# Optimization experiments

Hardware: AMD Instinct MI355X
Metric: run time of the kernel (lower is better)

The kernel has to match this reference:

```python
import jax, jax.numpy as jnp
import numpy as np

N = 20000; E = 320000; G = 64; C_IN = 128; H = 128; L = 3; S = 4
EPS = 1e-5; SLOPE = 0.01  # GraphNorm eps, leaky_relu negative slope


def _kruskal(ei, ew, n):
    # Kruskal MST over edges sorted by usage-count weight; returns bidirectional MST edges
    # and the updated usage counts (used edges get +1), mirroring kruskal_mst_track_usage.
    order = np.argsort(ew, kind='stable')
    s = ei[0][order]; d = ei[1][order]
    parent = np.arange(n)
    def find(u):
        while parent[u] != u:
            parent[u] = parent[parent[u]]
            u = parent[u]
        return u
    mst = []; used = []
    for i in range(s.shape[0]):
        ru = find(s[i]); rv = find(d[i])
        if ru != rv:
            parent[ru] = rv
            mst.append((s[i], d[i]))
            used.append(order[i])
            if len(mst) == n - 1:
                break
    ew = ew.copy(); ew[np.asarray(used)] += 1
    m = np.asarray(mst, dtype=np.int64).T  # [2, ~n-1]
    return np.concatenate([m, m[::-1]], axis=1), ew  # bidirectional


def setup_inputs():
    rng = np.random.default_rng(0)
    x = rng.standard_normal((N, C_IN), dtype=np.float32)
    edge_index = rng.integers(0, N, size=(2, E)).astype(np.int64)
    batch = np.sort(rng.integers(0, G, size=N)).astype(np.int64)
    # split_graph: shuffle edges, then repeatedly extract MSTs (no_grad / CPU in original)
    perm = rng.permutation(E)
    ei_p = edge_index[:, perm]
    ew = np.zeros(E, dtype=np.int64)
    msts = []
    for _ in range(S - 1):  # only splits 0..3 are used; split 0 is the shuffled full graph
        m, ew = _kruskal(ei_p, ew, N)
        msts.append(m)
    def gp(shape):
        return jnp.asarray((0.05 * rng.standard_normal(shape)).astype(np.float32))
    return {
        'x': jnp.asarray(x),
        'emb_W': gp((C_IN, H)), 'emb_b': gp((H,)),
        'main_W': gp((L, H, H)), 'main_b': gp((L, H)),
        'main_gw': jnp.ones((L, H), jnp.float32), 'main_gb': jnp.zeros((L, H), jnp.float32), 'main_gms': jnp.ones((L, H), jnp.float32),
        'loc_W': gp((L, H, H)), 'loc_b': gp((L, H)),
        'loc_gw': jnp.ones((L, H), jnp.float32), 'loc_gb': jnp.zeros((L, H), jnp.float32), 'loc_gms': jnp.ones((L, H), jnp.float32),
        'merge_W': gp((H * (S + 1), H)), 'merge_b': gp((H,)),
        'edge_index': jnp.asarray(edge_index),
        'edges0': jnp.asarray(ei_p),
        'edges1': jnp.asarray(msts[0]),
        'edges2': jnp.asarray(msts[1]),
        'edges3': jnp.asarray(msts[2]),
        'batch': jnp.asarray(batch),
    }


def _seg(v, idx, n):
    return jax.ops.segment_sum(v, idx, num_segments=n)


def _gcn(x, W, b, src, dst):
    # PyG GCNConv with self-loops and symmetric normalization
    n = x.shape[0]
    h = x @ W
    deg = _seg(jnp.ones(src.shape[0], x.dtype), dst, n) + 1.0
    dinv = jax.lax.rsqrt(deg)
    coef = (dinv[src] * dinv[dst])[:, None]
    out = _seg(h[src] * coef, dst, n) + h * (dinv * dinv)[:, None]  # neighbors + self-loop
    return out + b


def _graph_norm(x, batch, cnt, w, b, ms):
    # PyG GraphNorm: per-graph mean with learnable mean_scale, per-graph variance
    mean = _seg(x, batch, G) / cnt
    out = x - ms * mean[batch]
    var = _seg(out * out, batch, G) / cnt
    inv = jax.lax.rsqrt(var + EPS)
    return w * out * inv[batch] + b


def _gnn(x, src, dst, Ws, bs, gw, gb, gms, batch, cnt):
    hist = []
    for l in range(L):
        x = _gcn(x, Ws[l], bs[l], src, dst)
        x = _graph_norm(x, batch, cnt, gw[l], gb[l], gms[l])
        x = jax.nn.leaky_relu(x, SLOPE)
        hist.append(x)  # dropout in eval mode = identity
    return hist


def _forward(x, emb_W, emb_b, main_W, main_b, main_gw, main_gb, main_gms,
             loc_W, loc_b, loc_gw, loc_gb, loc_gms, merge_W, merge_b,
             edge_index, edges0, edges1, edges2, edges3, batch):
    cnt = jnp.maximum(_seg(jnp.ones(N, x.dtype), batch, G), 1.0)[:, None]  # [G,1]
    h = x @ emb_W + emb_b
    main_hist = _gnn(h, edge_index[0], edge_index[1], main_W, main_b, main_gw, main_gb, main_gms, batch, cnt)
    split_hists = [_gnn(h, e[0], e[1], loc_W, loc_b, loc_gw, loc_gb, loc_gms, batch, cnt)
                   for e in (edges0, edges1, edges2, edges3)]
    gs = []
    for l in range(L):
        xl = jnp.concatenate([sh[l] for sh in split_hists] + [main_hist[l]], axis=1)  # [N, 5H]
        xl = xl @ merge_W + merge_b
        gs.append(_seg(xl, batch, G) / cnt)  # global_mean_pool
    return jnp.mean(jnp.stack(gs), axis=0)  # [G, H]


def reference(x, emb_W, emb_b, main_W, main_b, main_gw, main_gb, main_gms,
              loc_W, loc_b, loc_gw, loc_gb, loc_gms, merge_W, merge_b,
              edge_index, edges0, edges1, edges2, edges3, batch):
    return _forward(x, emb_W, emb_b, main_W, main_b, main_gw, main_gb, main_gms,
                    loc_W, loc_b, loc_gw, loc_gb, loc_gms, merge_W, merge_b,
                    edge_index, edges0, edges1, edges2, edges3, batch)
```

## Files before the change

kernel.cpp:

```cpp
#include <hip/hip_runtime.h>

#define NN 20000
#define NNP 20032
#define NH 128
#define NG 64
#define NLAY 3
#define NCH 5
#define GEPS 1e-5f
#define GSLOPE 0.01f

typedef unsigned short u16;
typedef unsigned int u32;
typedef __attribute__((ext_vector_type(8))) short short8;
typedef __attribute__((ext_vector_type(4))) float float4v;
typedef __attribute__((ext_vector_type(2))) float f32x2;

__device__ __forceinline__ u16 f2bf(float f) {
  union { float f; u32 u; } v; v.f = f;
  u32 r = (v.u + 0x7fffu + ((v.u >> 16) & 1u)) >> 16;
  return (u16)r;
}

struct ZP {
  const u16* A[NCH];
  const u16* W[NCH];
  u16* Y[NCH];
  int ystride[NCH];
  u16* Xo[NCH];
  u16* Xn[NCH];
  const float* bias[NCH];
  const float* gw[NCH];
  const float* gb[NCH];
  const float* gms[NCH];
  int colbase[NCH];
};

struct ES4 {
  const int* e[4];
  int cnt[4];
  int off[4];
};


__global__ __launch_bounds__(1024) void k_scan(const int* __restrict__ deg,
                                               int* __restrict__ indptr,
                                               int* __restrict__ cursor,
                                               float* __restrict__ dinv,
                                               const int* __restrict__ batch,
                                               int* __restrict__ counts,
                                               int* __restrict__ gstart) {
  int s = blockIdx.x;
  int t = threadIdx.x;
  if (s == 4) {
    int g = t;
    if (g < NG) {
      auto lb = [&](int key) {
        int lo = 0, hi = NN;
        while (lo < hi) {
          int mid = (lo + hi) >> 1;
          if (batch[mid] < key) lo = mid + 1; else hi = mid;
        }
        return lo;
      };
      int a = lb(g), b = lb(g + 1);
      gstart[g] = a;
      counts[g] = b - a;
    }
    return;
  }
  const int* d = deg + s * NN;
  int* ip = indptr + s * (NN + 1);
  int* cu = cursor + s * (NN + 1);
  int lane = t & 63, wv = t >> 6;
  __shared__ int wsum[16];
  int run = 0;
  const int NT = (NN + 1023) / 1024;
  for (int tile = 0; tile < NT; tile++) {
    int idx = tile * 1024 + t;
    int v = 0;
    if (idx < NN) {
      v = d[idx];
      dinv[s * NN + idx] = rsqrtf((float)v + 1.0f);
    }
    int x = v;
#pragma unroll
    for (int o = 1; o < 64; o <<= 1) {
      int y = __shfl_up(x, o);
      if (lane >= o) x += y;
    }
    if (lane == 63) wsum[wv] = x;
    __syncthreads();
    if (wv == 0) {
      int y = (lane < 16) ? wsum[lane] : 0;
#pragma unroll
      for (int o = 1; o < 16; o <<= 1) {
        int z = __shfl_up(y, o);
        if (lane >= o) y += z;
      }
      if (lane < 16) wsum[lane] = y;
    }
    __syncthreads();
    int waveoff = (wv == 0) ? 0 : wsum[wv - 1];
    int excl = run + waveoff + x - v;
    if (idx < NN) { ip[idx] = excl; cu[idx] = excl; }
    run += wsum[15];
    __syncthreads();
  }
  if (t == 0) { ip[NN] = run; cu[NN] = run; }
}

__global__ void k_fill(ES4 es, const float* __restrict__ dinv, int* __restrict__ cursor,
                       u32* __restrict__ ent) {
  int s = blockIdx.y;
  int i = blockIdx.x * 256 + threadIdx.x;
  int E = es.cnt[s];
  if (i >= E) return;
  int src = es.e[s][i];
  int dst = es.e[s][E + i];
  int pos = atomicAdd(&cursor[s * (NN + 1) + dst], 1);
  float c = dinv[s * NN + src] * dinv[s * NN + dst];
  ent[es.off[s] + pos] = (u32)src | ((u32)f2bf(c) << 16);
}

__global__ __launch_bounds__(256) void k_setup(ES4 es, int* __restrict__ deg,
                                               const float* __restrict__ embW,
                                               const float* __restrict__ locW,
                                               const float* __restrict__ mainW,
                                               u16* __restrict__ wt,
                                               const float* __restrict__ x,
                                               u16* __restrict__ xb) {
  int ybk = blockIdx.y;
  if (ybk < 4) {
    int s = ybk;
    int i = blockIdx.x * 256 + threadIdx.x;
    int E = es.cnt[s];
    if (i < E) atomicAdd(&deg[s * NN + es.e[s][E + i]], 1);
    return;
  }
  if (ybk == 11) {
    int i = (blockIdx.x * 256 + threadIdx.x) * 8;
    if (i >= NN * NH) return;
    float4 a = *(const float4*)(x + i);
    float4 b = *(const float4*)(x + i + 4);
    uint4 o;
    o.x = f2bf(a.x) | ((u32)f2bf(a.y) << 16);
    o.y = f2bf(a.z) | ((u32)f2bf(a.w) << 16);
    o.z = f2bf(b.x) | ((u32)f2bf(b.y) << 16);
    o.w = f2bf(b.z) | ((u32)f2bf(b.w) << 16);
    *(uint4*)(xb + i) = o;
    return;
  }
  if (blockIdx.x >= 16) return;
  int mat = ybk - 4;
  const float* W = (mat == 0) ? embW : ((mat <= 3) ? locW + (mat - 1) * NH * NH
                                                   : mainW + (mat - 4) * NH * NH);
  int tile = blockIdx.x;
  int tk = (tile >> 2) * 32;
  int tn = (tile & 3) * 32;
  __shared__ float tl[32][33];
  int c = threadIdx.x & 31, r = threadIdx.x >> 5;
#pragma unroll
  for (int rr = 0; rr < 32; rr += 8)
    tl[r + rr][c] = W[(size_t)(tk + r + rr) * NH + tn + c];
  __syncthreads();
#pragma unroll
  for (int rr = 0; rr < 32; rr += 8)
    wt[(size_t)mat * NH * NH + (size_t)(tn + r + rr) * NH + tk + c] = f2bf(tl[c][r + rr]);
}


__global__ __launch_bounds__(256) void k_gemm_bf(ZP p, const float* __restrict__ gbias) {
  int zi = blockIdx.y;
  const u16* __restrict__ A = p.A[zi];
  const u16* __restrict__ Wt = p.W[zi];
  u16* __restrict__ Y = p.Y[zi];
  int yst = p.ystride[zi];
  __shared__ u16 As[64][136];
  __shared__ u16 Bs[128][136];
  int t = threadIdx.x;
  int row0 = blockIdx.x * 64;
  int c = t & 15, rs = t >> 4;
#pragma unroll
  for (int pass = 0; pass < 4; pass++) {
    int r = pass * 16 + rs;
    *(uint4*)(&As[r][c * 8]) = *(const uint4*)(A + (size_t)(row0 + r) * NH + c * 8);
  }
#pragma unroll
  for (int pass = 0; pass < 8; pass++) {
    int n = pass * 16 + rs;
    *(uint4*)(&Bs[n][c * 8]) = *(const uint4*)(Wt + (size_t)n * NH + c * 8);
  }
  __syncthreads();
  int lane = t & 63, w = t >> 6;
  int m16 = lane & 15, quad = lane >> 4;
  float4v acc[8];
#pragma unroll
  for (int i = 0; i < 8; i++) acc[i] = (float4v)(0.f);
#pragma unroll
  for (int kk = 0; kk < 4; kk++) {
    short8 av = *(const short8*)(&As[w * 16 + m16][kk * 32 + quad * 8]);
#pragma unroll
    for (int ct = 0; ct < 8; ct++) {
      short8 bv = *(const short8*)(&Bs[ct * 16 + m16][kk * 32 + quad * 8]);
      acc[ct] = __builtin_amdgcn_mfma_f32_16x16x32_bf16(av, bv, acc[ct], 0, 0, 0);
    }
  }
  __syncthreads();
#pragma unroll
  for (int ct = 0; ct < 8; ct++) {
    float bv = gbias ? gbias[ct * 16 + m16] : 0.f;
#pragma unroll
    for (int r = 0; r < 4; r++) {
      As[w * 16 + quad * 4 + r][ct * 16 + m16] = f2bf(acc[ct][r] + bv);
    }
  }
  __syncthreads();
#pragma unroll
  for (int pass = 0; pass < 4; pass++) {
    int r = pass * 16 + rs;
    int gr = row0 + r;
    if (gr < NN) *(uint4*)(Y + (size_t)gr * yst + c * 8) = *(const uint4*)(&As[r][c * 8]);
  }
}

__device__ __forceinline__ f32x2 bf2x2(u32 v) {
  f32x2 r;
  r.x = __uint_as_float(v << 16);
  r.y = __uint_as_float(v & 0xffff0000u);
  return r;
}

__device__ __forceinline__ void fma8p(f32x2* a, uint4 v, float cf) {
  f32x2 c2; c2.x = cf; c2.y = cf;
  a[0] += c2 * bf2x2(v.x);
  a[1] += c2 * bf2x2(v.y);
  a[2] += c2 * bf2x2(v.z);
  a[3] += c2 * bf2x2(v.w);
}

__device__ __forceinline__ void fin_chain(const float* a, const u16* Yb, int st, int node,
                                          int fo, float d2, const float* bias,
                                          u16* __restrict__ Xo) {
  uint4 sv = *(const uint4*)(Yb + (size_t)node * st + fo);
  float s[8] = {
    __uint_as_float(sv.x << 16), __uint_as_float(sv.x & 0xffff0000u),
    __uint_as_float(sv.y << 16), __uint_as_float(sv.y & 0xffff0000u),
    __uint_as_float(sv.z << 16), __uint_as_float(sv.z & 0xffff0000u),
    __uint_as_float(sv.w << 16), __uint_as_float(sv.w & 0xffff0000u)};
  float4 b0 = *(const float4*)(bias + fo);
  float4 b1 = *(const float4*)(bias + fo + 4);
  float bb[8] = {b0.x, b0.y, b0.z, b0.w, b1.x, b1.y, b1.z, b1.w};
  float o[8];
#pragma unroll
  for (int j = 0; j < 8; j++) o[j] = a[j] + d2 * s[j] + bb[j];
  uint4 ou;
  u32* op = (u32*)&ou;
#pragma unroll
  for (int j = 0; j < 4; j++)
    op[j] = (u32)f2bf(o[2 * j]) | ((u32)f2bf(o[2 * j + 1]) << 16);
  *(uint4*)(Xo + (size_t)node * NH + fo) = ou;
}

__global__ __launch_bounds__(256) void k_agg2(ZP p, const int* __restrict__ indptr,
                                              const u32* __restrict__ ent,
                                              const float* __restrict__ dinv, int4 entoff) {
  int b = blockIdx.x;
  int wv = threadIdx.x >> 6, lane = threadIdx.x & 63;
  int g = lane >> 4;
  int fo = (lane & 15) * 8;
  if (b < 5000) {
    int node = b * 4 + wv;
    int beg = indptr[node], end = indptr[node + 1];
    const u16* __restrict__ Y0 = p.Y[0];
    const u16* __restrict__ Y4 = p.Y[4];
    int st = p.ystride[0];
    f32x2 a0[4], a4[4];
#pragma unroll
    for (int j = 0; j < 4; j++) { a0[j] = (f32x2)(0.f); a4[j] = (f32x2)(0.f); }
    int e = beg + g;
    for (; e + 4 < end; e += 8) {
      u32 sa = ent[e];
      u32 sb = ent[e + 4];
      size_t ra = (size_t)(sa & 0xffffu) * st + fo;
      size_t rb = (size_t)(sb & 0xffffu) * st + fo;
      uint4 va0 = *(const uint4*)(Y0 + ra);
      uint4 va4 = *(const uint4*)(Y4 + ra);
      uint4 vb0 = *(const uint4*)(Y0 + rb);
      uint4 vb4 = *(const uint4*)(Y4 + rb);
      float ca = __uint_as_float(sa & 0xffff0000u);
      float cb = __uint_as_float(sb & 0xffff0000u);
      fma8p(a0, va0, ca); fma8p(a4, va4, ca);
      fma8p(a0, vb0, cb); fma8p(a4, vb4, cb);
    }
    if (e < end) {
      u32 sc = ent[e];
      float cf = __uint_as_float(sc & 0xffff0000u);
      size_t ro = (size_t)(sc & 0xffffu) * st + fo;
      uint4 v0 = *(const uint4*)(Y0 + ro);
      uint4 v4 = *(const uint4*)(Y4 + ro);
      fma8p(a0, v0, cf);
      fma8p(a4, v4, cf);
    }
    float* f0 = (float*)a0;
    float* f4 = (float*)a4;
#pragma unroll
    for (int j = 0; j < 8; j++) {
      f0[j] += __shfl_xor(f0[j], 16);
      f0[j] += __shfl_xor(f0[j], 32);
      f4[j] += __shfl_xor(f4[j], 16);
      f4[j] += __shfl_xor(f4[j], 32);
    }
    if (g == 0) {
      float di = dinv[node];
      float d2 = di * di;
      fin_chain(f0, Y0, st, node, fo, d2, p.bias[0], p.Xo[0]);
      fin_chain(f4, Y4, st, node, fo, d2, p.bias[4], p.Xo[4]);
    }
  } else {
    int mb = b - 5000;
    int s = 1 + mb / 1250;
    int node = (mb % 1250) * 16 + wv * 4 + g;
    const int* ip = indptr + s * (NN + 1);
    int eb = (s == 1) ? entoff.y : ((s == 2) ? entoff.z : entoff.w);
    const u16* __restrict__ Y = p.Y[s];
    int st = p.ystride[s];
    int beg = ip[node], end = ip[node + 1];
    const u32* __restrict__ ev = ent + eb;
    f32x2 a[4];
#pragma unroll
    for (int j = 0; j < 4; j++) a[j] = (f32x2)(0.f);
    for (int e = beg; e < end; e++) {
      u32 sc = ev[e];
      uint4 v = *(const uint4*)(Y + (size_t)(sc & 0xffffu) * st + fo);
      fma8p(a, v, __uint_as_float(sc & 0xffff0000u));
    }
    float di = dinv[s * NN + node];
    float d2 = di * di;
    fin_chain((float*)a, Y, st, node, fo, d2, p.bias[s], p.Xo[s]);
  }
}

__global__ __launch_bounds__(256) void k_norm2(ZP p, const int* __restrict__ gstart,
                                               const int* __restrict__ counts,
                                               float* __restrict__ Ml) {
  int g = blockIdx.x, zi = blockIdx.y, fc = blockIdx.z;
  const u16* __restrict__ X = p.Xo[zi];
  u16* __restrict__ Xn = p.Xn[zi];
  int t = threadIdx.x;
  int fj = t & 15;
  int f2 = fc * 32 + fj * 2;
  int rh = t >> 4;
  int start = gstart[g], cnt = counts[g];
  __shared__ float red[4][16][17];
  float s0 = 0.f, s1 = 0.f, q0 = 0.f, q1 = 0.f;
  for (int i = rh; i < cnt; i += 16) {
    u32 v = *(const u32*)(X + (size_t)(start + i) * NH + f2);
    float v0 = __uint_as_float(v << 16), v1 = __uint_as_float(v & 0xffff0000u);
    s0 += v0; q0 += v0 * v0;
    s1 += v1; q1 += v1 * v1;
  }
  red[0][rh][fj] = s0; red[1][rh][fj] = s1;
  red[2][rh][fj] = q0; red[3][rh][fj] = q1;
  __syncthreads();
#pragma unroll
  for (int off = 8; off >= 1; off >>= 1) {
    if (rh < off) {
      red[0][rh][fj] += red[0][rh + off][fj];
      red[1][rh][fj] += red[1][rh + off][fj];
      red[2][rh][fj] += red[2][rh + off][fj];
      red[3][rh][fj] += red[3][rh + off][fj];
    }
    __syncthreads();
  }
  float cntf = fmaxf((float)cnt, 1.f);
  float w0 = p.gw[zi][f2], w1 = p.gw[zi][f2 + 1];
  float b0 = p.gb[zi][f2], b1 = p.gb[zi][f2 + 1];
  float ms0 = p.gms[zi][f2], ms1 = p.gms[zi][f2 + 1];
  float mean0 = red[0][0][fj] / cntf, mean1 = red[1][0][fj] / cntf;
  float var0 = red[2][0][fj] / cntf - (2.f * ms0 - ms0 * ms0) * mean0 * mean0;
  float var1 = red[3][0][fj] / cntf - (2.f * ms1 - ms1 * ms1) * mean1 * mean1;
  float inv0 = rsqrtf(var0 + GEPS), inv1 = rsqrtf(var1 + GEPS);
  __syncthreads();
  float m0 = 0.f, m1 = 0.f;
  for (int i = rh; i < cnt; i += 16) {
    size_t ro = (size_t)(start + i) * NH + f2;
    u32 v = *(const u32*)(X + ro);
    float v0 = __uint_as_float(v << 16), v1 = __uint_as_float(v & 0xffff0000u);
    float o0 = w0 * (v0 - ms0 * mean0) * inv0 + b0;
    float o1 = w1 * (v1 - ms1 * mean1) * inv1 + b1;
    o0 = (o0 >= 0.f) ? o0 : GSLOPE * o0;
    o1 = (o1 >= 0.f) ? o1 : GSLOPE * o1;
    if (Xn) *(u32*)(Xn + ro) = (u32)f2bf(o0) | ((u32)f2bf(o1) << 16);
    m0 += o0; m1 += o1;
  }
  red[0][rh][fj] = m0; red[1][rh][fj] = m1;
  __syncthreads();
#pragma unroll
  for (int off = 8; off >= 1; off >>= 1) {
    if (rh < off) {
      red[0][rh][fj] += red[0][rh + off][fj];
      red[1][rh][fj] += red[1][rh + off][fj];
    }
    __syncthreads();
  }
  if (rh == 0) {
    int col = p.colbase[zi] + f2;
    Ml[(size_t)g * 640 + col] = red[0][0][fj];
    Ml[(size_t)g * 640 + col + 1] = red[1][0][fj];
  }
}

__global__ __launch_bounds__(256) void k_mergeout(const float* __restrict__ M,
                                                  const float* __restrict__ mergeW,
                                                  const float* __restrict__ mergeb,
                                                  const int* __restrict__ counts,
                                                  float* __restrict__ out) {
  int g = blockIdx.x;
  int f = threadIdx.x & 127, h = threadIdx.x >> 7;
  __shared__ float mrow[640];
  __shared__ float red[128];
  float acc = 0.f;
  for (int l = 0; l < NLAY; l++) {
    const float* Mr = M + ((size_t)l * NG + g) * 640;
    for (int i = threadIdx.x; i < 640; i += 256) mrow[i] = Mr[i];
    __syncthreads();
    float s = 0.f;
    int k0 = h * 320;
#pragma unroll 8
    for (int k = k0; k < k0 + 320; k++) s += mrow[k] * mergeW[(size_t)k * NH + f];
    if (h) red[f] = s;
    __syncthreads();
    if (!h) acc += s + red[f];
    __syncthreads();
  }
  if (!h) {
    float cnt = fmaxf((float)counts[g], 1.f);
    out[(size_t)g * NH + f] = acc / (3.f * cnt) + mergeb[f];
  }
}


struct Offs {
  size_t counts, gstart, deg, M, dinv, indptr, cursor, ent, wt, xbf, h0, ydual;
  size_t yb[NCH], xo[NCH], xn[NCH];
  size_t memset1_off, memset1_len, total;
};

static size_t build_offs(Offs& o, int Etot) {
  size_t off = 0;
  auto alloc = [&](size_t bytes) -> size_t {
    off = (off + 255) & ~(size_t)255;
    size_t s = off;
    off += bytes;
    return s;
  };
  o.counts = alloc(NG * 4);
  o.gstart = alloc(NG * 4);
  o.deg = alloc((size_t)4 * NN * 4);
  o.memset1_off = o.deg;
  o.memset1_len = (size_t)4 * NN * 4;
  o.M = alloc((size_t)NLAY * NG * 640 * 4);
  o.dinv = alloc((size_t)4 * NN * 4);
  o.indptr = alloc((size_t)4 * (NN + 1) * 4);
  o.cursor = alloc((size_t)4 * (NN + 1) * 4);
  o.ent = alloc((size_t)Etot * 4);
  o.wt = alloc((size_t)7 * NH * NH * 2);
  o.xbf = alloc((size_t)NNP * NH * 2);
  o.h0 = alloc((size_t)NNP * NH * 2);
  o.ydual = alloc((size_t)NN * 256 * 2);
  for (int i = 1; i < 4; i++) o.yb[i] = alloc((size_t)NN * NH * 2);
  for (int i = 0; i < NCH; i++) {
    o.xo[i] = alloc((size_t)NN * NH * 2);
    o.xn[i] = alloc((size_t)NNP * NH * 2);
  }
  o.total = off;
  return off;
}

extern "C" void kernel_launch(void* const* d_in, const int* in_sizes, int n_in,
                              void* d_out, int out_size, void* d_ws, size_t ws_size,
                              hipStream_t stream) {
  if (n_in < 21) return;
  const float* x = (const float*)d_in[0];
  const float* embW = (const float*)d_in[1];
  const float* embb = (const float*)d_in[2];
  const float* mainW = (const float*)d_in[3];
  const float* mainb = (const float*)d_in[4];
  const float* maingw = (const float*)d_in[5];
  const float* maingb = (const float*)d_in[6];
  const float* maingms = (const float*)d_in[7];
  const float* locW = (const float*)d_in[8];
  const float* locb = (const float*)d_in[9];
  const float* locgw = (const float*)d_in[10];
  const float* locgb = (const float*)d_in[11];
  const float* locgms = (const float*)d_in[12];
  const float* mergeW = (const float*)d_in[13];
  const float* mergeb = (const float*)d_in[14];
  const int* edge_index = (const int*)d_in[15];
  const int* edges1 = (const int*)d_in[17];
  const int* edges2 = (const int*)d_in[18];
  const int* edges3 = (const int*)d_in[19];
  const int* batch = (const int*)d_in[20];

  int E0 = in_sizes[15] / 2;
  int E1 = in_sizes[17] / 2, E2 = in_sizes[18] / 2, E3 = in_sizes[19] / 2;
  int Etot = E0 + E1 + E2 + E3;
  int maxE = E0 > E1 ? E0 : E1;
  maxE = maxE > E2 ? maxE : E2;
  maxE = maxE > E3 ? maxE : E3;

  Offs o;
  if (build_offs(o, Etot) > ws_size) return;

  char* ws = (char*)d_ws;
  int* counts = (int*)(ws + o.counts);
  int* gstart = (int*)(ws + o.gstart);
  int* deg = (int*)(ws + o.deg);
  float* M = (float*)(ws + o.M);
  float* dinv = (float*)(ws + o.dinv);
  int* indptr = (int*)(ws + o.indptr);
  int* cursor = (int*)(ws + o.cursor);
  u32* ent = (u32*)(ws + o.ent);
  u16* wt = (u16*)(ws + o.wt);
  u16* xbf = (u16*)(ws + o.xbf);
  u16* h0 = (u16*)(ws + o.h0);
  u16* ydual = (u16*)(ws + o.ydual);
  u16 *yb[NCH], *xo[NCH], *xn[NCH];
  for (int i = 1; i < 4; i++) yb[i] = (u16*)(ws + o.yb[i]);
  for (int i = 0; i < NCH; i++) {
    xo[i] = (u16*)(ws + o.xo[i]);
    xn[i] = (u16*)(ws + o.xn[i]);
  }

  ES4 es;
  es.e[0] = edge_index; es.e[1] = edges1; es.e[2] = edges2; es.e[3] = edges3;
  es.cnt[0] = E0; es.cnt[1] = E1; es.cnt[2] = E2; es.cnt[3] = E3;
  es.off[0] = 0; es.off[1] = E0; es.off[2] = E0 + E1; es.off[3] = E0 + E1 + E2;
  int4 entoff = make_int4(0, E0, E0 + E1, E0 + E1 + E2);

  hipMemsetAsync(ws + o.memset1_off, 0, o.memset1_len, stream);
  k_setup<<<dim3((maxE + 255) / 256, 12), 256, 0, stream>>>(es, deg, embW, locW, mainW,
                                                            wt, x, xbf);
  k_scan<<<5, 1024, 0, stream>>>(deg, indptr, cursor, dinv, batch, counts, gstart);
  k_fill<<<dim3((maxE + 255) / 256, 4), 256, 0, stream>>>(es, dinv, cursor, ent);

  const int nrb = (NN + 63) / 64;

  {
    ZP pe = {};
    pe.A[0] = xbf; pe.W[0] = wt; pe.Y[0] = h0; pe.ystride[0] = NH;
    k_gemm_bf<<<dim3(nrb, 1), 256, 0, stream>>>(pe, embb);
  }

  for (int l = 0; l < NLAY; l++) {
    ZP p = {};
    for (int zi = 0; zi < NCH; zi++) {
      bool isMain = (zi == 4);
      p.A[zi] = (l == 0) ? (const u16*)h0 : (const u16*)xn[zi];
      p.W[zi] = wt + (size_t)((isMain ? 4 : 1) + l) * NH * NH;
      if (zi == 0) { p.Y[0] = ydual; p.ystride[0] = 256; }
      else if (zi == 4) { p.Y[4] = ydual + 128; p.ystride[4] = 256; }
      else { p.Y[zi] = yb[zi]; p.ystride[zi] = 128; }
      p.Xo[zi] = xo[zi];
      p.Xn[zi] = (l == NLAY - 1) ? (u16*)nullptr : xn[zi];
      p.bias[zi] = (isMain ? mainb : locb) + (size_t)l * NH;
      p.gw[zi] = (isMain ? maingw : locgw) + (size_t)l * NH;
      p.gb[zi] = (isMain ? maingb : locgb) + (size_t)l * NH;
      p.gms[zi] = (isMain ? maingms : locgms) + (size_t)l * NH;
      p.colbase[zi] = isMain ? 512 : zi * NH;
    }
    if (l == 0) {
      ZP pg = {};
      pg.A[0] = h0; pg.W[0] = wt + (size_t)1 * NH * NH; pg.Y[0] = ydual; pg.ystride[0] = 256;
      pg.A[1] = h0; pg.W[1] = wt + (size_t)4 * NH * NH; pg.Y[1] = ydual + 128; pg.ystride[1] = 256;
      k_gemm_bf<<<dim3(nrb, 2), 256, 0, stream>>>(pg, (const float*)nullptr);
      p.Y[1] = ydual; p.Y[2] = ydual; p.Y[3] = ydual;
      p.ystride[1] = p.ystride[2] = p.ystride[3] = 256;
    } else {
      k_gemm_bf<<<dim3(nrb, NCH), 256, 0, stream>>>(p, (const float*)nullptr);
    }
    k_agg2<<<8750, 256, 0, stream>>>(p, indptr, ent, dinv, entoff);
    k_norm2<<<dim3(NG, NCH, 4), 256, 0, stream>>>(p, gstart, counts,
                                                  M + (size_t)l * NG * 640);
  }

  k_mergeout<<<NG, 256, 0, stream>>>(M, mergeW, mergeb, counts, (float*)d_out);
}
```

Measured before the change: 385.3 us.

## Fuse x bf16 conversion, embedding GEMM and layer-0 GEMMs into one kernel

Adds k_gemm0, which converts x to bf16 on load, runs the embedding GEMM with bias, keeps the resulting h in shared memory, and then runs the layer-0 local and main weight GEMMs from it, writing ydual directly. This removes the separate x-to-bf16 pass from k_setup, the h0 round trip through global memory and two kernel launches. In exchange each block now holds three 8-tile accumulator sets and reloads the weight tile twice, which may raise register pressure and lower occupancy.

```diff
diff --git a/kernel.cpp b/kernel.cpp
--- a/kernel.cpp
+++ b/kernel.cpp
@@ -126,28 +126,13 @@
                                                const float* __restrict__ embW,
                                                const float* __restrict__ locW,
                                                const float* __restrict__ mainW,
-                                               u16* __restrict__ wt,
-                                               const float* __restrict__ x,
-                                               u16* __restrict__ xb) {
+                                               u16* __restrict__ wt) {
   int ybk = blockIdx.y;
   if (ybk < 4) {
     int s = ybk;
     int i = blockIdx.x * 256 + threadIdx.x;
     int E = es.cnt[s];
     if (i < E) atomicAdd(&deg[s * NN + es.e[s][E + i]], 1);
-    return;
-  }
-  if (ybk == 11) {
-    int i = (blockIdx.x * 256 + threadIdx.x) * 8;
-    if (i >= NN * NH) return;
-    float4 a = *(const float4*)(x + i);
-    float4 b = *(const float4*)(x + i + 4);
-    uint4 o;
-    o.x = f2bf(a.x) | ((u32)f2bf(a.y) << 16);
-    o.y = f2bf(a.z) | ((u32)f2bf(a.w) << 16);
-    o.z = f2bf(b.x) | ((u32)f2bf(b.y) << 16);
-    o.w = f2bf(b.z) | ((u32)f2bf(b.w) << 16);
-    *(uint4*)(xb + i) = o;
     return;
   }
   if (blockIdx.x >= 16) return;
@@ -169,7 +154,123 @@
 }
 
 
-__global__ __launch_bounds__(256) void k_gemm_bf(ZP p, const float* __restrict__ gbias) {
+__global__ __launch_bounds__(256) void k_gemm0(const float* __restrict__ x,
+                                               const u16* __restrict__ wt,
+                                               const float* __restrict__ embb,
+                                               u16* __restrict__ ydual) {
+  __shared__ u16 As[64][136];
+  __shared__ u16 Bs[128][136];
+  int t = threadIdx.x;
+  int row0 = blockIdx.x * 64;
+  int c = t & 15, rs = t >> 4;
+#pragma unroll
+  for (int pass = 0; pass < 4; pass++) {
+    int r = pass * 16 + rs;
+    int gr = row0 + r;
+    uint4 o = make_uint4(0, 0, 0, 0);
+    if (gr < NN) {
+      float4 a = *(const float4*)(x + (size_t)gr * NH + c * 8);
+      float4 b = *(const float4*)(x + (size_t)gr * NH + c * 8 + 4);
+      o.x = f2bf(a.x) | ((u32)f2bf(a.y) << 16);
+      o.y = f2bf(a.z) | ((u32)f2bf(a.w) << 16);
+      o.z = f2bf(b.x) | ((u32)f2bf(b.y) << 16);
+      o.w = f2bf(b.z) | ((u32)f2bf(b.w) << 16);
+    }
+    *(uint4*)(&As[r][c * 8]) = o;
+  }
+#pragma unroll
+  for (int pass = 0; pass < 8; pass++) {
+    int n = pass * 16 + rs;
+    *(uint4*)(&Bs[n][c * 8]) = *(const uint4*)(wt + (size_t)n * NH + c * 8);
+  }
+  __syncthreads();
+  int lane = t & 63, w = t >> 6;
+  int m16 = lane & 15, quad = lane >> 4;
+  float4v acc[8];
+#pragma unroll
+  for (int i = 0; i < 8; i++) acc[i] = (float4v)(0.f);
+#pragma unroll
+  for (int kk = 0; kk < 4; kk++) {
+    short8 av = *(const short8*)(&As[w * 16 + m16][kk * 32 + quad * 8]);
+#pragma unroll
+    for (int ct = 0; ct < 8; ct++) {
+      short8 bv = *(const short8*)(&Bs[ct * 16 + m16][kk * 32 + quad * 8]);
+      acc[ct] = __builtin_amdgcn_mfma_f32_16x16x32_bf16(av, bv, acc[ct], 0, 0, 0);
+    }
+  }
+  __syncthreads();
+#pragma unroll
+  for (int ct = 0; ct < 8; ct++) {
+    float bv = embb[ct * 16 + m16];
+#pragma unroll
+    for (int r = 0; r < 4; r++)
+      As[w * 16 + quad * 4 + r][ct * 16 + m16] = f2bf(acc[ct][r] + bv);
+  }
+  {
+    const u16* wl = wt + (size_t)1 * NH * NH;
+#pragma unroll
+    for (int pass = 0; pass < 8; pass++) {
+      int n = pass * 16 + rs;
+      *(uint4*)(&Bs[n][c * 8]) = *(const uint4*)(wl + (size_t)n * NH + c * 8);
+    }
+  }
+  __syncthreads();
+  float4v acc0[8];
+#pragma unroll
+  for (int i = 0; i < 8; i++) acc0[i] = (float4v)(0.f);
+#pragma unroll
+  for (int kk = 0; kk < 4; kk++) {
+    short8 av = *(const short8*)(&As[w * 16 + m16][kk * 32 + quad * 8]);
+#pragma unroll
+    for (int ct = 0; ct < 8; ct++) {
+      short8 bv = *(const short8*)(&Bs[ct * 16 + m16][kk * 32 + quad * 8]);
+      acc0[ct] = __builtin_amdgcn_mfma_f32_16x16x32_bf16(av, bv, acc0[ct], 0, 0, 0);
+    }
+  }
+  __syncthreads();
+  {
+    const u16* wm = wt + (size_t)4 * NH * NH;
+#pragma unroll
+    for (int pass = 0; pass < 8; pass++) {
+      int n = pass * 16 + rs;
+      *(uint4*)(&Bs[n][c * 8]) = *(const uint4*)(wm + (size_t)n * NH + c * 8);
+    }
+  }
+  __syncthreads();
+  float4v acc4[8];
+#pragma unroll
+  for (int i = 0; i < 8; i++) acc4[i] = (float4v)(0.f);
+#pragma unroll
+  for (int kk = 0; kk < 4; kk++) {
+    short8 av = *(const short8*)(&As[w * 16 + m16][kk * 32 + quad * 8]);
+#pragma unroll
+    for (int ct = 0; ct < 8; ct++) {
+      short8 bv = *(const short8*)(&Bs[ct * 16 + m16][kk * 32 + quad * 8]);
+      acc4[ct] = __builtin_amdgcn_mfma_f32_16x16x32_bf16(av, bv, acc4[ct], 0, 0, 0);
+    }
+  }
+  __syncthreads();
+#pragma unroll
+  for (int ct = 0; ct < 8; ct++) {
+#pragma unroll
+    for (int r = 0; r < 4; r++) {
+      As[w * 16 + quad * 4 + r][ct * 16 + m16] = f2bf(acc0[ct][r]);
+      Bs[w * 16 + quad * 4 + r][ct * 16 + m16] = f2bf(acc4[ct][r]);
+    }
+  }
+  __syncthreads();
+#pragma unroll
+  for (int pass = 0; pass < 4; pass++) {
+    int r = pass * 16 + rs;
+    int gr = row0 + r;
+    if (gr < NN) {
+      *(uint4*)(ydual + (size_t)gr * 256 + c * 8) = *(const uint4*)(&As[r][c * 8]);
+      *(uint4*)(ydual + (size_t)gr * 256 + 128 + c * 8) = *(const uint4*)(&Bs[r][c * 8]);
+    }
+  }
+}
+
+__global__ __launch_bounds__(256) void k_gemm_bf(ZP p) {
   int zi = blockIdx.y;
   const u16* __restrict__ A = p.A[zi];
   const u16* __restrict__ Wt = p.W[zi];
@@ -208,10 +309,9 @@
   __syncthreads();
 #pragma unroll
   for (int ct = 0; ct < 8; ct++) {
-    float bv = gbias ? gbias[ct * 16 + m16] : 0.f;
 #pragma unroll
     for (int r = 0; r < 4; r++) {
-      As[w * 16 + quad * 4 + r][ct * 16 + m16] = f2bf(acc[ct][r] + bv);
+      As[w * 16 + quad * 4 + r][ct * 16 + m16] = f2bf(acc[ct][r]);
     }
   }
   __syncthreads();
@@ -441,7 +541,7 @@
 
 
 struct Offs {
-  size_t counts, gstart, deg, M, dinv, indptr, cursor, ent, wt, xbf, h0, ydual;
+  size_t counts, gstart, deg, M, dinv, indptr, cursor, ent, wt, ydual;
   size_t yb[NCH], xo[NCH], xn[NCH];
   size_t memset1_off, memset1_len, total;
 };
@@ -465,8 +565,6 @@
   o.cursor = alloc((size_t)4 * (NN + 1) * 4);
   o.ent = alloc((size_t)Etot * 4);
   o.wt = alloc((size_t)7 * NH * NH * 2);
-  o.xbf = alloc((size_t)NNP * NH * 2);
-  o.h0 = alloc((size_t)NNP * NH * 2);
   o.ydual = alloc((size_t)NN * 256 * 2);
   for (int i = 1; i < 4; i++) o.yb[i] = alloc((size_t)NN * NH * 2);
   for (int i = 0; i < NCH; i++) {
@@ -522,8 +620,6 @@
   int* cursor = (int*)(ws + o.cursor);
   u32* ent = (u32*)(ws + o.ent);
   u16* wt = (u16*)(ws + o.wt);
-  u16* xbf = (u16*)(ws + o.xbf);
-  u16* h0 = (u16*)(ws + o.h0);
   u16* ydual = (u16*)(ws + o.ydual);
   u16 *yb[NCH], *xo[NCH], *xn[NCH];
   for (int i = 1; i < 4; i++) yb[i] = (u16*)(ws + o.yb[i]);
@@ -539,24 +635,19 @@
   int4 entoff = make_int4(0, E0, E0 + E1, E0 + E1 + E2);
 
   hipMemsetAsync(ws + o.memset1_off, 0, o.memset1_len, stream);
-  k_setup<<<dim3((maxE + 255) / 256, 12), 256, 0, stream>>>(es, deg, embW, locW, mainW,
-                                                            wt, x, xbf);
+  k_setup<<<dim3((maxE + 255) / 256, 11), 256, 0, stream>>>(es, deg, embW, locW, mainW, wt);
   k_scan<<<5, 1024, 0, stream>>>(deg, indptr, cursor, dinv, batch, counts, gstart);
   k_fill<<<dim3((maxE + 255) / 256, 4), 256, 0, stream>>>(es, dinv, cursor, ent);
 
   const int nrb = (NN + 63) / 64;
 
-  {
-    ZP pe = {};
-    pe.A[0] = xbf; pe.W[0] = wt; pe.Y[0] = h0; pe.ystride[0] = NH;
-    k_gemm_bf<<<dim3(nrb, 1), 256, 0, stream>>>(pe, embb);
-  }
+  k_gemm0<<<nrb, 256, 0, stream>>>(x, wt, embb, ydual);
 
   for (int l = 0; l < NLAY; l++) {
     ZP p = {};
     for (int zi = 0; zi < NCH; zi++) {
       bool isMain = (zi == 4);
-      p.A[zi] = (l == 0) ? (const u16*)h0 : (const u16*)xn[zi];
+      p.A[zi] = (const u16*)xn[zi];
       p.W[zi] = wt + (size_t)((isMain ? 4 : 1) + l) * NH * NH;
       if (zi == 0) { p.Y[0] = ydual; p.ystride[0] = 256; }
       else if (zi == 4) { p.Y[4] = ydual + 128; p.ystride[4] = 256; }
@@ -570,14 +661,10 @@
       p.colbase[zi] = isMain ? 512 : zi * NH;
     }
     if (l == 0) {
-      ZP pg = {};
-      pg.A[0] = h0; pg.W[0] = wt + (size_t)1 * NH * NH; pg.Y[0] = ydual; pg.ystride[0] = 256;
-      pg.A[1] = h0; pg.W[1] = wt + (size_t)4 * NH * NH; pg.Y[1] = ydual + 128; pg.ystride[1] = 256;
-      k_gemm_bf<<<dim3(nrb, 2), 256, 0, stream>>>(pg, (const float*)nullptr);
       p.Y[1] = ydual; p.Y[2] = ydual; p.Y[3] = ydual;
       p.ystride[1] = p.ystride[2] = p.ystride[3] = 256;
     } else {
-      k_gemm_bf<<<dim3(nrb, NCH), 256, 0, stream>>>(p, (const float*)nullptr);
+      k_gemm_bf<<<dim3(nrb, NCH), 256, 0, stream>>>(p);
     }
     k_agg2<<<8750, 256, 0, stream>>>(p, indptr, ent, dinv, entoff);
     k_norm2<<<dim3(NG, NCH, 4), 256, 0, stream>>>(p, gstart, counts,
```

New measurement: 381.0 us, median of 2. Within noise of the previous version (-1.1%).
